# Performance work log

Measured on AMD Instinct MI355X. Metric: run time of the kernel, lower is better.

Reference implementation:

```python
import jax, jax.numpy as jnp
import numpy as np

B, N, D, H = 8, 1024, 1024, 16
DH = D // H
REL_VOCAB = 6  # stadia + 2
NEG_INF = -1e9


def setup_inputs() -> dict:
    key = jax.random.key(0)
    ks = jax.random.split(key, 8)
    hid = jax.random.normal(ks[0], (B, N, D), dtype=jnp.float32)
    adj = jax.random.randint(ks[1], (B, N, N), 0, 2, dtype=jnp.int32)
    relative_pos = jax.random.randint(ks[2], (B, N, N), 0, REL_VOCAB, dtype=jnp.int32)
    s = 1.0 / np.sqrt(D)
    Wq = jax.random.normal(ks[3], (D, D), dtype=jnp.float32) * s
    Wk = jax.random.normal(ks[4], (D, D), dtype=jnp.float32) * s
    Wv = jax.random.normal(ks[5], (D, D), dtype=jnp.float32) * s
    rel_table = jax.random.normal(ks[6], (REL_VOCAB, 1), dtype=jnp.float32)
    ln_gamma = jnp.ones((D,), dtype=jnp.float32)
    ln_beta = jnp.zeros((D,), dtype=jnp.float32)
    return {"hid": hid, "adj": adj, "relative_pos": relative_pos,
            "Wq": Wq, "Wk": Wk, "Wv": Wv, "rel_table": rel_table,
            "ln_gamma": ln_gamma, "ln_beta": ln_beta}


def _layer_norm(x, gamma, beta, eps=1e-5):
    mu = jnp.mean(x, axis=-1, keepdims=True)
    var = jnp.var(x, axis=-1, keepdims=True)
    return (x - mu) * jax.lax.rsqrt(var + eps) * gamma + beta


def reference(hid, adj, relative_pos, Wq, Wk, Wv, rel_table, ln_gamma, ln_beta):
    # relative position bias: embedding dim 1, squeezed -> [B, N, N]
    rel_bias = rel_table[relative_pos][..., 0]
    # projections, split into heads: [B, N, H, DH]
    q = (hid @ Wq).reshape(B, N, H, DH)
    k = (hid @ Wk).reshape(B, N, H, DH)
    v = (hid @ Wv).reshape(B, N, H, DH)
    # scores [B, H, N, N], scaled by sqrt(key_dim) = sqrt(D)
    scores = jnp.einsum('bqhd,bkhd->bhqk', q, k) / jnp.sqrt(jnp.float32(D))
    scores = scores + rel_bias[:, None, :, :]
    mask = (adj != 0)[:, None, :, :]
    scores = jnp.where(mask, scores, NEG_INF)
    attn = jax.nn.softmax(scores, axis=-1)
    out = jnp.einsum('bhqk,bkhd->bqhd', attn, v).reshape(B, N, D)
    out = jax.nn.relu(out) + hid  # activation + residual
    return _layer_norm(out, ln_gamma, ln_beta)
```

## Files before the change

kernel.cpp:

```cpp
#include <hip/hip_runtime.h>
#include <math.h>

#define Bc 8
#define Nc 1024
#define Dc 1024
#define Hc 16
#define DHc 64
#define NEGINF -1e9f

typedef unsigned int  u32;
typedef unsigned short u16;
typedef unsigned long long u64;
typedef u16  u16x8 __attribute__((ext_vector_type(8)));
typedef u16  u16x4 __attribute__((ext_vector_type(4)));
typedef __bf16 bf16x8 __attribute__((ext_vector_type(8)));
typedef float f32x4 __attribute__((ext_vector_type(4)));

__device__ __forceinline__ u16 f2bf(float f) {
    u32 u = __builtin_bit_cast(u32, f);
    u += 0x7fffu + ((u >> 16) & 1u);
    return (u16)(u >> 16);
}
__device__ __forceinline__ float bf2f(u16 b) {
    return __builtin_bit_cast(float, (u32)b << 16);
}
__device__ __forceinline__ u32 pack2bf(float lo, float hi) {
    return __builtin_amdgcn_perm(__builtin_bit_cast(u32, hi),
                                 __builtin_bit_cast(u32, lo), 0x07060302u);
}

__device__ __forceinline__ void glds16(const u16* g, const u16* l) {
    __builtin_amdgcn_global_load_lds(
        (const __attribute__((address_space(1))) void*)(u64)g,
        (__attribute__((address_space(3))) void*)(u32)(u64)l, 16, 0, 0);
}

__global__ __launch_bounds__(256) void bias_prep(
    const int* __restrict__ adj, const int* __restrict__ relpos,
    const float* __restrict__ rel_table, u16* __restrict__ bias)
{
    __shared__ float tbl[8];
    int t = threadIdx.x;
    if (t < 6) tbl[t] = rel_table[t];
    __syncthreads();
    int i = blockIdx.x * 256 + t;
    int pos4 = i << 2;
    int row  = pos4 >> 10;
    int p    = pos4 & 1023;
    int blk  = p & ~63;
    int m    = (p & 63) >> 2;
    size_t base = ((size_t)row << 10) + blk + m;
    u16x4 o;
#pragma unroll
    for (int j = 0; j < 4; ++j) {
        int a  = adj[base + 16 * j];
        int rp = relpos[base + 16 * j];
        o[j] = a ? f2bf(tbl[rp]) : f2bf(NEGINF);
    }
    ((u16x4*)bias)[i] = o;
}

__global__ __launch_bounds__(256) void hid2bf(const float* __restrict__ in,
                                              u16* __restrict__ out)
{
    int idx = blockIdx.x * 256 + threadIdx.x;
    float4 a = ((const float4*)in)[2 * idx];
    float4 b = ((const float4*)in)[2 * idx + 1];
    u16x8 o;
    o[0] = f2bf(a.x); o[1] = f2bf(a.y); o[2] = f2bf(a.z); o[3] = f2bf(a.w);
    o[4] = f2bf(b.x); o[5] = f2bf(b.y); o[6] = f2bf(b.z); o[7] = f2bf(b.w);
    ((u16x8*)out)[idx] = o;
}

__global__ __launch_bounds__(256) void wtrans(
    const float* __restrict__ Wq, const float* __restrict__ Wk,
    const float* __restrict__ Wv, u16* __restrict__ WqT,
    u16* __restrict__ WkT, u16* __restrict__ WvT)
{
    const float* W; u16* WT;
    if (blockIdx.z == 0)      { W = Wq; WT = WqT; }
    else if (blockIdx.z == 1) { W = Wk; WT = WkT; }
    else                      { W = Wv; WT = WvT; }
    __shared__ float tile[32][33];
    int tx = threadIdx.x, ty = threadIdx.y;
    int n0 = blockIdx.x * 32, k0 = blockIdx.y * 32;
#pragma unroll
    for (int i = 0; i < 4; ++i) {
        int r = ty + i * 8;
        tile[r][tx] = W[(size_t)(k0 + r) * Dc + n0 + tx];
    }
    __syncthreads();
#pragma unroll
    for (int i = 0; i < 4; ++i) {
        int n = ty + i * 8;
        WT[(size_t)(n0 + n) * Dc + k0 + tx] = f2bf(tile[tx][n]);
    }
}

__global__ __launch_bounds__(256) void qkv_mfma(
    const u16* __restrict__ hidb, const u16* __restrict__ WqT,
    const u16* __restrict__ WkT, const u16* __restrict__ WvT,
    u16* __restrict__ qo, u16* __restrict__ ko, u16* __restrict__ vo)
{
    __shared__ u16 As[128 * 64];
    __shared__ u16 Bs[128 * 64];

    const int bx = blockIdx.x, by = blockIdx.y;
    const int z = bx >> 3;
    const int c0 = (bx << 7) & 1023;
    const int row0 = by << 7;
    const u16* WT; u16* out;
    if (z == 0)      { WT = WqT; out = qo; }
    else if (z == 1) { WT = WkT; out = ko; }
    else             { WT = WvT; out = vo; }

    const int tid = threadIdx.x;
    const int wave = tid >> 6, lane = tid & 63;
    const int g = lane >> 4, li = lane & 15;
    const int wr = wave >> 1, wc = wave & 1;
    const int lr = lane >> 3, ls = lane & 7;
    const int sseg = ls ^ lr;

    const u16* pa = hidb + (size_t)(row0 + wave * 32 + lr) * Dc + sseg * 8;
    const u16* pb = WT   + (size_t)(c0   + wave * 32 + lr) * Dc + sseg * 8;
    u16* la = &As[(wave * 32) * 64];
    u16* lb = &Bs[(wave * 32) * 64];

    f32x4 acc[4][4] = {};

    const int swz = (li & 7);

    for (int kt = 0; kt < Dc; kt += 64) {
        __syncthreads();
#pragma unroll
        for (int i = 0; i < 4; ++i) {
            glds16(pa + kt + i * 8 * Dc, la + i * 8 * 64);
            glds16(pb + kt + i * 8 * Dc, lb + i * 8 * 64);
        }
        __syncthreads();
#pragma unroll
        for (int ks = 0; ks < 2; ++ks) {
            const int soff = ((ks * 4 + g) ^ swz) * 8;
            bf16x8 af[4], bf[4];
#pragma unroll
            for (int mi = 0; mi < 4; ++mi)
                af[mi] = *(const bf16x8*)&As[(wr * 64 + mi * 16 + li) * 64 + soff];
#pragma unroll
            for (int nj = 0; nj < 4; ++nj)
                bf[nj] = *(const bf16x8*)&Bs[(wc * 64 + nj * 16 + li) * 64 + soff];
#pragma unroll
            for (int mi = 0; mi < 4; ++mi)
#pragma unroll
                for (int nj = 0; nj < 4; ++nj)
                    acc[mi][nj] = __builtin_amdgcn_mfma_f32_16x16x32_bf16(
                        af[mi], bf[nj], acc[mi][nj], 0, 0, 0);
        }
    }

    const int b = row0 >> 10;

    if (z != 2) {
        const int nbase = (row0 & 1023) + wr * 64 + g * 4;
#pragma unroll
        for (int mi = 0; mi < 4; ++mi)
#pragma unroll
            for (int rr = 0; rr < 4; ++rr) {
                int n = nbase + mi * 16 + rr;
#pragma unroll
                for (int nj = 0; nj < 4; ++nj) {
                    int cz = c0 + wc * 64 + nj * 16 + li;
                    out[(((size_t)(b * Hc + (cz >> 6)) * Nc + n) * DHc) + (cz & 63)]
                        = f2bf(acc[mi][nj][rr]);
                }
            }
    } else {
        __syncthreads();
        u16* T = ((wave & 2) ? Bs : As) + (wave & 1) * 4096;
#pragma unroll
        for (int mi = 0; mi < 4; ++mi)
#pragma unroll
            for (int rr = 0; rr < 4; ++rr) {
                int r = mi * 16 + g * 4 + rr;
                int pp = ((r & 15) << 2) | (r >> 4);
#pragma unroll
                for (int nj = 0; nj < 4; ++nj) {
                    int c = nj * 16 + li;
                    T[c * 64 + ((((pp >> 3) ^ (c & 7)) << 3) | (pp & 7))]
                        = f2bf(acc[mi][nj][rr]);
                }
            }
        const int nseg = ls ^ lr;
#pragma unroll
        for (int i = 0; i < 8; ++i) {
            int cl = i * 8 + lr;
            u16x8 val = *(const u16x8*)&T[cl * 64 + ls * 8];
            int cz = c0 + wc * 64 + cl;
            int n = (row0 & 1023) + wr * 64 + nseg * 8;
            *(u16x8*)&out[(((size_t)(b * Hc + (cz >> 6)) * DHc + (cz & 63)) * Nc) + n] = val;
        }
    }
}

__global__ __launch_bounds__(256, 4) void attn_mfma(
    const u16* __restrict__ q, const u16* __restrict__ k,
    const u16* __restrict__ v, const u16* __restrict__ bias,
    float* __restrict__ attn_out)
{
    __shared__ u16 Ks[64 * 64];
    __shared__ u16 VTs[64 * 64];
    __shared__ u16 PQ[128 * 72];

    const int tid = threadIdx.x;
    const int w = tid >> 6, lane = tid & 63;
    const int g = lane >> 4, li = lane & 15;
    const int lr8 = lane >> 3, ls8 = lane & 7;
    const int lseg = ls8 ^ lr8;

    const int id = blockIdx.x;
    const int p  = (id & 7) | ((id >> 6) << 3);
    const int qt = (id >> 3) & 7;
    const int b = p >> 4, h = p & 15;
    const int q0 = qt << 7;

    {
        const int sr = tid >> 1;
        const int sh = (tid & 1) * 32;
        const u16* qp = q + ((size_t)((b * Hc + h) * Nc) + q0 + sr) * DHc + sh;
        u16x8 a0 = *(const u16x8*)qp;
        u16x8 a1 = *(const u16x8*)(qp + 8);
        u16x8 a2 = *(const u16x8*)(qp + 16);
        u16x8 a3 = *(const u16x8*)(qp + 24);
        u16* dst = &PQ[sr * 72 + sh];
        *(u16x8*)(dst)      = a0; *(u16x8*)(dst + 8)  = a1;
        *(u16x8*)(dst + 16) = a2; *(u16x8*)(dst + 24) = a3;
    }
    __syncthreads();

    bf16x8 qf[2][2];
#pragma unroll
    for (int mt = 0; mt < 2; ++mt)
#pragma unroll
        for (int ks = 0; ks < 2; ++ks)
            qf[mt][ks] = *(const bf16x8*)&PQ[(w * 32 + mt * 16 + li) * 72 + ks * 32 + g * 8];

    f32x4 o_[2][4] = {};
    float lsum[2][4] = {};

    const float scale = 0.03125f;
    const u16* kbase = k + (size_t)(b * Hc + h) * Nc * DHc;
    const u16* vbase = v + (size_t)(b * Hc + h) * DHc * Nc;
    const u16* brow  = bias + ((size_t)(b * Nc) + q0 + w * 32) * Nc + 4 * li;

    for (int k0 = 0; k0 < Nc; k0 += 64) {
        __syncthreads();
        {
            const u16* kp = kbase + (size_t)(k0 + w * 16 + lr8) * DHc + lseg * 8;
            const u16* vp = vbase + (size_t)(w * 16 + lr8) * Nc + k0 + lseg * 8;
            u16* kl = &Ks[(w * 16) * 64];
            u16* vl = &VTs[(w * 16) * 64];
            glds16(kp,           kl);
            glds16(kp + 8 * DHc, kl + 8 * 64);
            glds16(vp,           vl);
            glds16(vp + 8 * Nc,  vl + 8 * 64);
        }
        u16x4 brv[2][4];
#pragma unroll
        for (int mt = 0; mt < 2; ++mt)
#pragma unroll
            for (int r = 0; r < 4; ++r)
                brv[mt][r] = *(const u16x4*)&brow[(size_t)(mt * 16 + g * 4 + r) * Nc + k0];
        __syncthreads();

        f32x4 sacc[2][4] = {};
#pragma unroll
        for (int ks = 0; ks < 2; ++ks) {
            const int so = (((ks << 2) | g) ^ (li & 7)) << 3;
#pragma unroll
            for (int nt = 0; nt < 4; ++nt) {
                bf16x8 kf = *(const bf16x8*)&Ks[(nt * 16 + li) * 64 + so];
                sacc[0][nt] = __builtin_amdgcn_mfma_f32_16x16x32_bf16(qf[0][ks], kf, sacc[0][nt], 0, 0, 0);
                sacc[1][nt] = __builtin_amdgcn_mfma_f32_16x16x32_bf16(qf[1][ks], kf, sacc[1][nt], 0, 0, 0);
            }
        }

#pragma unroll
        for (int mt = 0; mt < 2; ++mt)
#pragma unroll
            for (int r = 0; r < 4; ++r) {
                const int qrl = mt * 16 + g * 4 + r;
                float pv[4];
#pragma unroll
                for (int nt = 0; nt < 4; ++nt) {
                    float sv = sacc[mt][nt][r] * scale + bf2f(brv[mt][r][nt]);
                    pv[nt] = __expf(sv);
                    lsum[mt][r] += pv[nt];
                }
                u32* dst = (u32*)&PQ[(w * 32 + qrl) * 72 + li * 4];
                dst[0] = pack2bf(pv[0], pv[1]);
                dst[1] = pack2bf(pv[2], pv[3]);
            }

#pragma unroll
        for (int ks = 0; ks < 2; ++ks) {
            const int so = (((ks << 2) | g) ^ (li & 7)) << 3;
            bf16x8 pa0 = *(const bf16x8*)&PQ[(w * 32 + li) * 72 + ks * 32 + g * 8];
            bf16x8 pa1 = *(const bf16x8*)&PQ[(w * 32 + 16 + li) * 72 + ks * 32 + g * 8];
#pragma unroll
            for (int j = 0; j < 4; ++j) {
                bf16x8 vf = *(const bf16x8*)&VTs[(j * 16 + li) * 64 + so];
                o_[0][j] = __builtin_amdgcn_mfma_f32_16x16x32_bf16(pa0, vf, o_[0][j], 0, 0, 0);
                o_[1][j] = __builtin_amdgcn_mfma_f32_16x16x32_bf16(pa1, vf, o_[1][j], 0, 0, 0);
            }
        }
    }

#pragma unroll
    for (int mt = 0; mt < 2; ++mt)
#pragma unroll
        for (int r = 0; r < 4; ++r) {
            float l = lsum[mt][r];
            l += __shfl_xor(l, 1);
            l += __shfl_xor(l, 2);
            l += __shfl_xor(l, 4);
            l += __shfl_xor(l, 8);
            float inv = 1.f / l;
            int qrow = q0 + w * 32 + mt * 16 + g * 4 + r;
            float* op = attn_out + ((size_t)b * Nc + qrow) * Dc + h * DHc;
#pragma unroll
            for (int j = 0; j < 4; ++j)
                op[j * 16 + li] = o_[mt][j][r] * inv;
        }
}

__global__ __launch_bounds__(256) void ln_kernel(
    const float* attn_out, const float* __restrict__ hid,
    const float* __restrict__ gamma, const float* __restrict__ beta,
    float* out)
{
    const int row = blockIdx.x;
    const int t = threadIdx.x;

    float4 av = *(const float4*)&attn_out[(size_t)row * Dc + t * 4];
    float4 hv = *(const float4*)&hid[(size_t)row * Dc + t * 4];
    float x0 = fmaxf(av.x, 0.f) + hv.x;
    float x1 = fmaxf(av.y, 0.f) + hv.y;
    float x2 = fmaxf(av.z, 0.f) + hv.z;
    float x3 = fmaxf(av.w, 0.f) + hv.w;

    float s1 = x0 + x1 + x2 + x3;
    float s2 = x0 * x0 + x1 * x1 + x2 * x2 + x3 * x3;
#pragma unroll
    for (int off = 1; off < 64; off <<= 1) {
        s1 += __shfl_xor(s1, off);
        s2 += __shfl_xor(s2, off);
    }
    __shared__ float w1[4], w2[4];
    int lane = t & 63, wid = t >> 6;
    if (lane == 0) { w1[wid] = s1; w2[wid] = s2; }
    __syncthreads();
    s1 = w1[0] + w1[1] + w1[2] + w1[3];
    s2 = w2[0] + w2[1] + w2[2] + w2[3];

    float mu  = s1 * (1.f / 1024.f);
    float var = s2 * (1.f / 1024.f) - mu * mu;
    float rstd = rsqrtf(var + 1e-5f);

    float4 g  = *(const float4*)&gamma[t * 4];
    float4 be = *(const float4*)&beta[t * 4];
    float4 r4;
    r4.x = (x0 - mu) * rstd * g.x + be.x;
    r4.y = (x1 - mu) * rstd * g.y + be.y;
    r4.z = (x2 - mu) * rstd * g.z + be.z;
    r4.w = (x3 - mu) * rstd * g.w + be.w;
    *(float4*)&out[(size_t)row * Dc + t * 4] = r4;
}

extern "C" void kernel_launch(void* const* d_in, const int* in_sizes, int n_in,
                              void* d_out, int out_size, void* d_ws, size_t ws_size,
                              hipStream_t stream) {
    const float* hid       = (const float*)d_in[0];
    const int*   adj       = (const int*)d_in[1];
    const int*   relpos    = (const int*)d_in[2];
    const float* Wq        = (const float*)d_in[3];
    const float* Wk        = (const float*)d_in[4];
    const float* Wv        = (const float*)d_in[5];
    const float* rel_table = (const float*)d_in[6];
    const float* gamma     = (const float*)d_in[7];
    const float* beta      = (const float*)d_in[8];
    float* out = (float*)d_out;

    const size_t per  = (size_t)Bc * Hc * Nc * DHc;
    const size_t wsz  = (size_t)Dc * Dc;
    u16* qb   = (u16*)d_ws;
    u16* kb   = qb + per;
    u16* vb   = kb + per;
    u16* bias = vb + per;
    u16* hidb = bias + (size_t)Bc * Nc * Nc;
    u16* wqT  = hidb + (size_t)Bc * Nc * Dc;
    u16* wkT  = wqT + wsz;
    u16* wvT  = wkT + wsz;

    bias_prep<<<(Bc * Nc * Nc) / (4 * 256), 256, 0, stream>>>(adj, relpos, rel_table, bias);
    hid2bf<<<(Bc * Nc * Dc) / (8 * 256), 256, 0, stream>>>(hid, hidb);
    wtrans<<<dim3(32, 32, 3), dim3(32, 8), 0, stream>>>(Wq, Wk, Wv, wqT, wkT, wvT);
    qkv_mfma<<<dim3(24, 64), 256, 0, stream>>>(hidb, wqT, wkT, wvT, qb, kb, vb);
    attn_mfma<<<1024, 256, 0, stream>>>(qb, kb, vb, bias, out);
    ln_kernel<<<Bc * Nc, 256, 0, stream>>>(out, hid, gamma, beta, out);
}
```

Before: 298.3 us.

## Double-buffer K/V tiles in attention, fuse prep kernels, pack Q/K stores

The attention kernel now double-buffers its K and V shared-memory tiles and prefetches the next bias slice into registers, so global-to-LDS loads overlap with MFMA work and one barrier per iteration is removed. Its launch-bounds occupancy hint drops from 4 to 3 to make room for the extra LDS and registers. The three preprocessing kernels (bias build, hid to bf16, weight transpose) are merged into one launch split by block index to save launch overhead. The Q/K epilogue writes four packed bf16 values per store instead of scattered 16-bit stores, which also reorders columns within each head consistently for Q and K.

```diff
diff --git a/kernel.cpp b/kernel.cpp
--- a/kernel.cpp
+++ b/kernel.cpp
@@ -13,6 +13,7 @@
 typedef unsigned long long u64;
 typedef u16  u16x8 __attribute__((ext_vector_type(8)));
 typedef u16  u16x4 __attribute__((ext_vector_type(4)));
+typedef u32  u32x2 __attribute__((ext_vector_type(2)));
 typedef __bf16 bf16x8 __attribute__((ext_vector_type(8)));
 typedef float f32x4 __attribute__((ext_vector_type(4)));
 
@@ -35,65 +36,65 @@
         (__attribute__((address_space(3))) void*)(u32)(u64)l, 16, 0, 0);
 }
 
-__global__ __launch_bounds__(256) void bias_prep(
+__global__ __launch_bounds__(256) void prep_fused(
     const int* __restrict__ adj, const int* __restrict__ relpos,
-    const float* __restrict__ rel_table, u16* __restrict__ bias)
-{
-    __shared__ float tbl[8];
-    int t = threadIdx.x;
-    if (t < 6) tbl[t] = rel_table[t];
-    __syncthreads();
-    int i = blockIdx.x * 256 + t;
-    int pos4 = i << 2;
-    int row  = pos4 >> 10;
-    int p    = pos4 & 1023;
-    int blk  = p & ~63;
-    int m    = (p & 63) >> 2;
-    size_t base = ((size_t)row << 10) + blk + m;
-    u16x4 o;
-#pragma unroll
-    for (int j = 0; j < 4; ++j) {
-        int a  = adj[base + 16 * j];
-        int rp = relpos[base + 16 * j];
-        o[j] = a ? f2bf(tbl[rp]) : f2bf(NEGINF);
-    }
-    ((u16x4*)bias)[i] = o;
-}
-
-__global__ __launch_bounds__(256) void hid2bf(const float* __restrict__ in,
-                                              u16* __restrict__ out)
-{
-    int idx = blockIdx.x * 256 + threadIdx.x;
-    float4 a = ((const float4*)in)[2 * idx];
-    float4 b = ((const float4*)in)[2 * idx + 1];
-    u16x8 o;
-    o[0] = f2bf(a.x); o[1] = f2bf(a.y); o[2] = f2bf(a.z); o[3] = f2bf(a.w);
-    o[4] = f2bf(b.x); o[5] = f2bf(b.y); o[6] = f2bf(b.z); o[7] = f2bf(b.w);
-    ((u16x8*)out)[idx] = o;
-}
-
-__global__ __launch_bounds__(256) void wtrans(
+    const float* __restrict__ rel_table, u16* __restrict__ bias,
+    const float* __restrict__ hid, u16* __restrict__ hidb,
     const float* __restrict__ Wq, const float* __restrict__ Wk,
     const float* __restrict__ Wv, u16* __restrict__ WqT,
     u16* __restrict__ WkT, u16* __restrict__ WvT)
 {
-    const float* W; u16* WT;
-    if (blockIdx.z == 0)      { W = Wq; WT = WqT; }
-    else if (blockIdx.z == 1) { W = Wk; WT = WkT; }
-    else                      { W = Wv; WT = WvT; }
-    __shared__ float tile[32][33];
-    int tx = threadIdx.x, ty = threadIdx.y;
-    int n0 = blockIdx.x * 32, k0 = blockIdx.y * 32;
-#pragma unroll
-    for (int i = 0; i < 4; ++i) {
-        int r = ty + i * 8;
-        tile[r][tx] = W[(size_t)(k0 + r) * Dc + n0 + tx];
-    }
-    __syncthreads();
-#pragma unroll
-    for (int i = 0; i < 4; ++i) {
-        int n = ty + i * 8;
-        WT[(size_t)(n0 + n) * Dc + k0 + tx] = f2bf(tile[tx][n]);
+    const int blk = blockIdx.x;
+    const int t = threadIdx.x;
+
+    if (blk < 8192) {
+        __shared__ float tbl[8];
+        if (t < 6) tbl[t] = rel_table[t];
+        __syncthreads();
+        int i = blk * 256 + t;
+        int pos4 = i << 2;
+        int row  = pos4 >> 10;
+        int p    = pos4 & 1023;
+        int blkb = p & ~63;
+        int m    = (p & 63) >> 2;
+        size_t base = ((size_t)row << 10) + blkb + m;
+        u16x4 o;
+#pragma unroll
+        for (int j = 0; j < 4; ++j) {
+            int a  = adj[base + 16 * j];
+            int rp = relpos[base + 16 * j];
+            o[j] = a ? f2bf(tbl[rp]) : f2bf(NEGINF);
+        }
+        ((u16x4*)bias)[i] = o;
+    } else if (blk < 12288) {
+        int idx = (blk - 8192) * 256 + t;
+        float4 a = ((const float4*)hid)[2 * idx];
+        float4 b = ((const float4*)hid)[2 * idx + 1];
+        u16x8 o;
+        o[0] = f2bf(a.x); o[1] = f2bf(a.y); o[2] = f2bf(a.z); o[3] = f2bf(a.w);
+        o[4] = f2bf(b.x); o[5] = f2bf(b.y); o[6] = f2bf(b.z); o[7] = f2bf(b.w);
+        ((u16x8*)hidb)[idx] = o;
+    } else {
+        __shared__ float tile[32][33];
+        const int wb = blk - 12288;
+        const int x = wb & 31, y = (wb >> 5) & 31, z = wb >> 10;
+        const float* W; u16* WT;
+        if (z == 0)      { W = Wq; WT = WqT; }
+        else if (z == 1) { W = Wk; WT = WkT; }
+        else             { W = Wv; WT = WvT; }
+        const int tx = t & 31, ty = t >> 5;
+        const int n0 = x * 32, k0 = y * 32;
+#pragma unroll
+        for (int i = 0; i < 4; ++i) {
+            int r = ty + i * 8;
+            tile[r][tx] = W[(size_t)(k0 + r) * Dc + n0 + tx];
+        }
+        __syncthreads();
+#pragma unroll
+        for (int i = 0; i < 4; ++i) {
+            int n = ty + i * 8;
+            WT[(size_t)(n0 + n) * Dc + k0 + tx] = f2bf(tile[tx][n]);
+        }
     }
 }
 
@@ -160,18 +161,17 @@
     const int b = row0 >> 10;
 
     if (z != 2) {
+        const int h2 = (c0 + wc * 64) >> 6;
         const int nbase = (row0 & 1023) + wr * 64 + g * 4;
 #pragma unroll
         for (int mi = 0; mi < 4; ++mi)
 #pragma unroll
             for (int rr = 0; rr < 4; ++rr) {
                 int n = nbase + mi * 16 + rr;
-#pragma unroll
-                for (int nj = 0; nj < 4; ++nj) {
-                    int cz = c0 + wc * 64 + nj * 16 + li;
-                    out[(((size_t)(b * Hc + (cz >> 6)) * Nc + n) * DHc) + (cz & 63)]
-                        = f2bf(acc[mi][nj][rr]);
-                }
+                u32x2 pk;
+                pk.x = (u32)f2bf(acc[mi][0][rr]) | ((u32)f2bf(acc[mi][1][rr]) << 16);
+                pk.y = (u32)f2bf(acc[mi][2][rr]) | ((u32)f2bf(acc[mi][3][rr]) << 16);
+                *(u32x2*)(out + ((size_t)(b * Hc + h2) * Nc + n) * DHc + 4 * li) = pk;
             }
     } else {
         __syncthreads();
@@ -201,13 +201,13 @@
     }
 }
 
-__global__ __launch_bounds__(256, 4) void attn_mfma(
+__global__ __launch_bounds__(256, 3) void attn_mfma(
     const u16* __restrict__ q, const u16* __restrict__ k,
     const u16* __restrict__ v, const u16* __restrict__ bias,
     float* __restrict__ attn_out)
 {
-    __shared__ u16 Ks[64 * 64];
-    __shared__ u16 VTs[64 * 64];
+    __shared__ u16 Ks[2][64 * 64];
+    __shared__ u16 VTs[2][64 * 64];
     __shared__ u16 PQ[128 * 72];
 
     const int tid = threadIdx.x;
@@ -221,6 +221,20 @@
     const int qt = (id >> 3) & 7;
     const int b = p >> 4, h = p & 15;
     const int q0 = qt << 7;
+
+    const float scale = 0.03125f;
+    const u16* kbase = k + (size_t)(b * Hc + h) * Nc * DHc;
+    const u16* vbase = v + (size_t)(b * Hc + h) * DHc * Nc;
+    const u16* brow  = bias + ((size_t)(b * Nc) + q0 + w * 32) * Nc + 4 * li;
+
+    {
+        const u16* kp = kbase + (size_t)(w * 16 + lr8) * DHc + lseg * 8;
+        const u16* vp = vbase + (size_t)(w * 16 + lr8) * Nc + lseg * 8;
+        glds16(kp,           &Ks[0][(w * 16) * 64]);
+        glds16(kp + 8 * DHc, &Ks[0][(w * 16) * 64 + 8 * 64]);
+        glds16(vp,           &VTs[0][(w * 16) * 64]);
+        glds16(vp + 8 * Nc,  &VTs[0][(w * 16) * 64 + 8 * 64]);
+    }
 
     {
         const int sr = tid >> 1;
@@ -234,7 +248,13 @@
         *(u16x8*)(dst)      = a0; *(u16x8*)(dst + 8)  = a1;
         *(u16x8*)(dst + 16) = a2; *(u16x8*)(dst + 24) = a3;
     }
-    __syncthreads();
+
+    u16x4 brv[2][4];
+#pragma unroll
+    for (int mt = 0; mt < 2; ++mt)
+#pragma unroll
+        for (int r = 0; r < 4; ++r)
+            brv[mt][r] = *(const u16x4*)&brow[(size_t)(mt * 16 + g * 4 + r) * Nc];
 
     bf16x8 qf[2][2];
 #pragma unroll
@@ -246,30 +266,27 @@
     f32x4 o_[2][4] = {};
     float lsum[2][4] = {};
 
-    const float scale = 0.03125f;
-    const u16* kbase = k + (size_t)(b * Hc + h) * Nc * DHc;
-    const u16* vbase = v + (size_t)(b * Hc + h) * DHc * Nc;
-    const u16* brow  = bias + ((size_t)(b * Nc) + q0 + w * 32) * Nc + 4 * li;
-
-    for (int k0 = 0; k0 < Nc; k0 += 64) {
-        __syncthreads();
-        {
-            const u16* kp = kbase + (size_t)(k0 + w * 16 + lr8) * DHc + lseg * 8;
-            const u16* vp = vbase + (size_t)(w * 16 + lr8) * Nc + k0 + lseg * 8;
-            u16* kl = &Ks[(w * 16) * 64];
-            u16* vl = &VTs[(w * 16) * 64];
+    for (int it = 0; it < 16; ++it) {
+        const int cur = it & 1;
+        __syncthreads();
+
+        u16x4 brn[2][4];
+        if (it < 15) {
+            const int k1 = (it + 1) * 64;
+            const u16* kp = kbase + (size_t)(k1 + w * 16 + lr8) * DHc + lseg * 8;
+            const u16* vp = vbase + (size_t)(w * 16 + lr8) * Nc + k1 + lseg * 8;
+            u16* kl = &Ks[cur ^ 1][(w * 16) * 64];
+            u16* vl = &VTs[cur ^ 1][(w * 16) * 64];
             glds16(kp,           kl);
             glds16(kp + 8 * DHc, kl + 8 * 64);
             glds16(vp,           vl);
             glds16(vp + 8 * Nc,  vl + 8 * 64);
-        }
-        u16x4 brv[2][4];
-#pragma unroll
-        for (int mt = 0; mt < 2; ++mt)
-#pragma unroll
-            for (int r = 0; r < 4; ++r)
-                brv[mt][r] = *(const u16x4*)&brow[(size_t)(mt * 16 + g * 4 + r) * Nc + k0];
-        __syncthreads();
+#pragma unroll
+            for (int mt = 0; mt < 2; ++mt)
+#pragma unroll
+                for (int r = 0; r < 4; ++r)
+                    brn[mt][r] = *(const u16x4*)&brow[(size_t)(mt * 16 + g * 4 + r) * Nc + k1];
+        }
 
         f32x4 sacc[2][4] = {};
 #pragma unroll
@@ -277,7 +294,7 @@
             const int so = (((ks << 2) | g) ^ (li & 7)) << 3;
 #pragma unroll
             for (int nt = 0; nt < 4; ++nt) {
-                bf16x8 kf = *(const bf16x8*)&Ks[(nt * 16 + li) * 64 + so];
+                bf16x8 kf = *(const bf16x8*)&Ks[cur][(nt * 16 + li) * 64 + so];
                 sacc[0][nt] = __builtin_amdgcn_mfma_f32_16x16x32_bf16(qf[0][ks], kf, sacc[0][nt], 0, 0, 0);
                 sacc[1][nt] = __builtin_amdgcn_mfma_f32_16x16x32_bf16(qf[1][ks], kf, sacc[1][nt], 0, 0, 0);
             }
@@ -307,10 +324,18 @@
             bf16x8 pa1 = *(const bf16x8*)&PQ[(w * 32 + 16 + li) * 72 + ks * 32 + g * 8];
 #pragma unroll
             for (int j = 0; j < 4; ++j) {
-                bf16x8 vf = *(const bf16x8*)&VTs[(j * 16 + li) * 64 + so];
+                bf16x8 vf = *(const bf16x8*)&VTs[cur][(j * 16 + li) * 64 + so];
                 o_[0][j] = __builtin_amdgcn_mfma_f32_16x16x32_bf16(pa0, vf, o_[0][j], 0, 0, 0);
                 o_[1][j] = __builtin_amdgcn_mfma_f32_16x16x32_bf16(pa1, vf, o_[1][j], 0, 0, 0);
             }
+        }
+
+        if (it < 15) {
+#pragma unroll
+            for (int mt = 0; mt < 2; ++mt)
+#pragma unroll
+                for (int r = 0; r < 4; ++r)
+                    brv[mt][r] = brn[mt][r];
         }
     }
 
@@ -400,9 +425,8 @@
     u16* wkT  = wqT + wsz;
     u16* wvT  = wkT + wsz;
 
-    bias_prep<<<(Bc * Nc * Nc) / (4 * 256), 256, 0, stream>>>(adj, relpos, rel_table, bias);
-    hid2bf<<<(Bc * Nc * Dc) / (8 * 256), 256, 0, stream>>>(hid, hidb);
-    wtrans<<<dim3(32, 32, 3), dim3(32, 8), 0, stream>>>(Wq, Wk, Wv, wqT, wkT, wvT);
+    prep_fused<<<15360, 256, 0, stream>>>(adj, relpos, rel_table, bias,
+                                          hid, hidb, Wq, Wk, Wv, wqT, wkT, wvT);
     qkv_mfma<<<dim3(24, 64), 256, 0, stream>>>(hidb, wqT, wkT, wvT, qb, kb, vb);
     attn_mfma<<<1024, 256, 0, stream>>>(qb, kb, vb, bias, out);
     ln_kernel<<<Bc * Nc, 256, 0, stream>>>(out, hid, gamma, beta, out);
```

New measurement: 289.2 us. 1.03x faster.
